# Optimization experiments

Hardware: AMD Instinct MI355X
Metric: run time of the kernel (lower is better)

Reference implementation:

```python
import jax, jax.numpy as jnp
import numpy as np

B, T, H = 4, 2048, 1024
NH = 16
HD = H // NH  # 64
NEG_INF = -1.0e9  # module uses -1e9, not -inf


def setup_inputs() -> dict:
    key = jax.random.key(0)
    k1, k2, k3 = jax.random.split(key, 3)
    x = jax.random.normal(k1, (B, T, H), dtype=jnp.float32)
    W_qkv = jax.random.normal(k2, (3 * H, H), dtype=jnp.float32) * (1.0 / np.sqrt(H))
    W_out = jax.random.normal(k3, (H, H), dtype=jnp.float32) * (1.0 / np.sqrt(H))
    return {"x": x, "W_qkv": W_qkv, "W_out": W_out}


def reference(x, W_qkv, W_out):
    Bx, Tx, C = x.shape
    qkv = x @ W_qkv.T                              # [B,T,3H]
    q, k, v = jnp.split(qkv, 3, axis=-1)
    # [B,T,H] -> [B,NH,T,HD]
    q = q.reshape(Bx, Tx, NH, HD).transpose(0, 2, 1, 3)
    k = k.reshape(Bx, Tx, NH, HD).transpose(0, 2, 1, 3)
    v = v.reshape(Bx, Tx, NH, HD).transpose(0, 2, 1, 3)
    scale = 1.0 / np.sqrt(HD)
    scores = jnp.einsum('bhqd,bhkd->bhqk', q, k) * scale  # [B,NH,T,T]
    causal = jnp.tril(jnp.ones((Tx, Tx), dtype=bool))[None, None]
    scores = jnp.where(causal, scores, jnp.asarray(NEG_INF, scores.dtype))
    attn = jax.nn.softmax(scores, axis=-1)
    out = jnp.einsum('bhqk,bhkd->bhqd', attn, v)   # [B,NH,T,HD]
    out = out.transpose(0, 2, 1, 3).reshape(Bx, Tx, C)
    return out @ W_out.T
```

## Files before the change

### kernel.cpp

```cpp
#include <hip/hip_runtime.h>
#include <hip/hip_bf16.h>


typedef unsigned short ushort_t;
typedef __attribute__((ext_vector_type(8))) short  s8v;
typedef __attribute__((ext_vector_type(4))) float  f4v;
typedef __attribute__((ext_vector_type(4))) unsigned int u4v;

__device__ inline ushort_t f2bf(float f) {
    unsigned u = __builtin_bit_cast(unsigned, f);
    u += 0x7fffu + ((u >> 16) & 1u);
    return (ushort_t)(u >> 16);
}

__device__ inline void gload16(const ushort_t* g, ushort_t* l) {
    __builtin_amdgcn_global_load_lds(
        (const __attribute__((address_space(1))) unsigned int*)g,
        (__attribute__((address_space(3))) unsigned int*)l, 16, 0, 0);
}

__global__ __launch_bounds__(256) void cast_f32_bf16(
    const float* __restrict__ in, ushort_t* __restrict__ out, int n8)
{
    int i = blockIdx.x * 256 + threadIdx.x;
    if (i >= n8) return;
    const float* p = in + (size_t)i * 8;
    f4v a = *(const f4v*)p;
    f4v b = *(const f4v*)(p + 4);
    union { u4v v; ushort_t u[8]; } o;
    #pragma unroll
    for (int j = 0; j < 4; j++) { o.u[j] = f2bf(a[j]); o.u[j + 4] = f2bf(b[j]); }
    *(u4v*)(out + (size_t)i * 8) = o.v;
}

__global__ __launch_bounds__(256) void transpose_v(
    const ushort_t* __restrict__ in, ushort_t* __restrict__ out)
{
    const int t0 = blockIdx.x * 64;
    const int bh = blockIdx.y;
    const ushort_t* src = in  + ((size_t)bh * 2048 + t0) * 64;
    ushort_t*       dst = out + (size_t)bh * 64 * 2048 + t0;
    __shared__ __align__(16) ushort_t L[64 * 72];
    const int tid = threadIdx.x;

    #pragma unroll
    for (int j = 0; j < 2; j++) {
        int c = tid + j * 256;
        int t = c >> 3, d0 = (c & 7) * 8;
        *(s8v*)&L[t * 72 + d0] = *(const s8v*)(src + (size_t)t * 64 + d0);
    }
    __syncthreads();
    #pragma unroll
    for (int j = 0; j < 2; j++) {
        int c = tid + j * 256;
        int d = c >> 3, sp0 = (c & 7) * 8;
        union { s8v v; ushort_t u[8]; } o;
        #pragma unroll
        for (int i = 0; i < 8; i++) {
            int sp = sp0 + i;
            int sl = sp & 31;
            int k  = (sp >> 5) * 32 + (sl & 1) * 16 + (sl >> 1);
            o.u[i] = L[k * 72 + d];
        }
        *(s8v*)(dst + (size_t)d * 2048 + sp0) = o.v;
    }
}

template<int MODE>
__global__ __launch_bounds__(256) void gemm_nt(
    const ushort_t* __restrict__ A, const ushort_t* __restrict__ Bm,
    ushort_t* __restrict__ o0, ushort_t* __restrict__ o1, ushort_t* __restrict__ o2,
    float* __restrict__ of)
{
    __shared__ __align__(16) ushort_t As[2][4096];
    __shared__ __align__(16) ushort_t Bs[2][4096];

    const int tid  = threadIdx.x;
    const int m0   = blockIdx.x * 128;
    const int n0   = blockIdx.y * 128;
    const int wave = tid >> 6, lane = tid & 63;
    const int wr = wave >> 1, wc = wave & 1;
    const int lhi = lane >> 4, llo = lane & 15;
    const int srow = lane >> 2;
    const int scol = (((lane & 3) ^ ((srow >> 1) & 3)) * 8);

    auto stage = [&](int k0, int buf) {
        #pragma unroll
        for (int p = 0; p < 2; p++) {
            int chunk = wave * 2 + p;
            int row = chunk * 16 + srow;
            gload16(A  + (size_t)(m0 + row) * 1024 + k0 + scol,
                    &As[buf][chunk * 512 + lane * 8]);
            gload16(Bm + (size_t)(n0 + row) * 1024 + k0 + scol,
                    &Bs[buf][chunk * 512 + lane * 8]);
        }
    };

    f4v acc[4][4] = {};
    int buf = 0;

    stage(0, 0);
    __syncthreads();

    for (int k0 = 0; k0 < 1024; k0 += 32) {
        if (k0 + 32 < 1024) stage(k0 + 32, buf ^ 1);

        const int rch = (lhi ^ ((llo >> 1) & 3)) * 8;
        s8v a[4], b[4];
        #pragma unroll
        for (int i = 0; i < 4; i++)
            a[i] = *(const s8v*)&As[buf][(wr * 64 + i * 16 + llo) * 32 + rch];
        #pragma unroll
        for (int i = 0; i < 4; i++)
            b[i] = *(const s8v*)&Bs[buf][(wc * 64 + i * 16 + llo) * 32 + rch];
        #pragma unroll
        for (int i = 0; i < 4; i++)
            #pragma unroll
            for (int j = 0; j < 4; j++)
                acc[i][j] = __builtin_amdgcn_mfma_f32_16x16x32_bf16(a[i], b[j], acc[i][j], 0, 0, 0);

        __syncthreads();
        buf ^= 1;
    }

    #pragma unroll
    for (int i = 0; i < 4; i++) {
        #pragma unroll
        for (int j = 0; j < 4; j++) {
            #pragma unroll
            for (int r = 0; r < 4; r++) {
                int m = m0 + wr * 64 + i * 16 + lhi * 4 + r;
                int n = n0 + wc * 64 + j * 16 + llo;
                if (MODE == 1) {
                    of[(size_t)m * 1024 + n] = acc[i][j][r];
                } else {
                    float val = acc[i][j][r];
                    int b  = m >> 11, t = m & 2047;
                    int which = n >> 10, hh = n & 1023;
                    int head = hh >> 6, d = hh & 63;
                    size_t bh = (size_t)(b * 16 + head);
                    if (which == 0)
                        o0[(size_t)m * 1024 + hh] = f2bf(val * 0.18033688011112042f);
                    else {
                        ushort_t* dst = (which == 1) ? o1 : o2;
                        dst[(bh * 2048 + t) * 64 + d] = f2bf(val);
                    }
                }
            }
        }
    }
}

__global__ __launch_bounds__(512, 4) void attn_kernel(
    const ushort_t* __restrict__ q_ws, const ushort_t* __restrict__ k_ws,
    const ushort_t* __restrict__ v_ws, ushort_t* __restrict__ ao_ws)
{
    const int p    = blockIdx.x;
    const int bh   = blockIdx.y;
    const int tid  = threadIdx.x;
    const int wave = tid >> 6, lane = tid & 63;
    const int lhi = lane >> 4, llo = lane & 15;
    const int b = bh >> 4, head = bh & 15;

    const ushort_t* Kb = k_ws + (size_t)bh * 2048 * 64;
    const ushort_t* Vb = v_ws + (size_t)bh * 64 * 2048;

    __shared__ __align__(16) ushort_t Ks [2][4096];
    __shared__ __align__(16) ushort_t Vts[2][4096];
    __shared__ __align__(16) ushort_t Ps [8][2][1280];

    const int srow = wave * 8 + (lane >> 3);
    const int gch  = ((lane & 7) ^ (srow & 7)) * 8;
    auto stage = [&](int t, int buf) {
        const int kk0 = t * 64;
        gload16(Kb + (size_t)(kk0 + srow) * 64 + gch,
                &Ks[buf][srow * 64 + (lane & 7) * 8]);
        gload16(Vb + (size_t)srow * 2048 + kk0 + gch,
                &Vts[buf][srow * 64 + (lane & 7) * 8]);
    };

    const int qt  = (wave >> 2) ? (15 - p) : p;
    const int wq0 = qt * 128 + (wave & 3) * 32;

    s8v qf[2][2];
    #pragma unroll
    for (int g = 0; g < 2; g++) {
        const ushort_t* Qp = q_ws + (size_t)(b * 2048 + wq0 + g * 16 + llo) * 1024 + head * 64;
        qf[g][0] = *(const s8v*)(Qp + lhi * 8);
        qf[g][1] = *(const s8v*)(Qp + 32 + lhi * 8);
    }

    f4v o[2][4] = {};
    float lsum[2][4] = {};

    const int ntb = 32 - 2 * p;
    const int xs  = llo & 7;
    int cur = 0;

    stage(0, 0);
    __syncthreads();

    #pragma unroll 1
    for (int t = 0; t < ntb; t++) {
        if (t + 1 < ntb) stage(t + 1, cur ^ 1);

        const int kk0 = t * 64;
        if (kk0 <= wq0 + 31) {
            f4v s0[4], s1[4];
            #pragma unroll
            for (int c = 0; c < 4; c++) {
                const int rb = (c * 16 + llo) * 64;
                s8v kb0 = *(const s8v*)&Ks[cur][rb + ((lhi    ) ^ xs) * 8];
                s8v kb1 = *(const s8v*)&Ks[cur][rb + ((4 + lhi) ^ xs) * 8];
                f4v z0 = {}, z1 = {};
                z0 = __builtin_amdgcn_mfma_f32_16x16x32_bf16(qf[0][0], kb0, z0, 0, 0, 0);
                z0 = __builtin_amdgcn_mfma_f32_16x16x32_bf16(qf[0][1], kb1, z0, 0, 0, 0);
                z1 = __builtin_amdgcn_mfma_f32_16x16x32_bf16(qf[1][0], kb0, z1, 0, 0, 0);
                z1 = __builtin_amdgcn_mfma_f32_16x16x32_bf16(qf[1][1], kb1, z1, 0, 0, 0);
                s0[c] = z0; s1[c] = z1;
            }

            #pragma unroll
            for (int g = 0; g < 2; g++) {
                const int qrb = wq0 + g * 16;
                f4v* s = g ? s1 : s0;
                if ((kk0 + 63) > qrb) {
                    #pragma unroll
                    for (int c = 0; c < 4; c++) {
                        int kkg = kk0 + c * 16 + llo;
                        #pragma unroll
                        for (int r = 0; r < 4; r++)
                            if (kkg > qrb + lhi * 4 + r) s[c][r] = -1e9f;
                    }
                }
                #pragma unroll
                for (int h = 0; h < 2; h++) {
                    #pragma unroll
                    for (int r = 0; r < 4; r++) {
                        float p0 = __builtin_amdgcn_exp2f(s[2 * h][r]);
                        float p1 = __builtin_amdgcn_exp2f(s[2 * h + 1][r]);
                        lsum[g][r] += p0 + p1;
                        unsigned pk;
                        asm("v_cvt_pk_bf16_f32 %0, %1, %2" : "=v"(pk) : "v"(p0), "v"(p1));
                        *(unsigned*)&Ps[wave][g][h * 640 + (lhi * 4 + r) * 40 + llo * 2] = pk;
                    }
                }
            }

            s8v pa[2][2];
            #pragma unroll
            for (int g = 0; g < 2; g++) {
                pa[g][0] = *(const s8v*)&Ps[wave][g][llo * 40 + lhi * 8];
                pa[g][1] = *(const s8v*)&Ps[wave][g][640 + llo * 40 + lhi * 8];
            }
            #pragma unroll
            for (int cd = 0; cd < 4; cd++) {
                const int rb = (cd * 16 + llo) * 64;
                s8v vb0 = *(const s8v*)&Vts[cur][rb + ((lhi    ) ^ xs) * 8];
                s8v vb1 = *(const s8v*)&Vts[cur][rb + ((4 + lhi) ^ xs) * 8];
                #pragma unroll
                for (int g = 0; g < 2; g++) {
                    o[g][cd] = __builtin_amdgcn_mfma_f32_16x16x32_bf16(pa[g][0], vb0, o[g][cd], 0, 0, 0);
                    o[g][cd] = __builtin_amdgcn_mfma_f32_16x16x32_bf16(pa[g][1], vb1, o[g][cd], 0, 0, 0);
                }
            }
        }

        __syncthreads();
        cur ^= 1;
    }

    #pragma unroll
    for (int off = 1; off < 16; off <<= 1)
        #pragma unroll
        for (int g = 0; g < 2; g++)
            #pragma unroll
            for (int r = 0; r < 4; r++)
                lsum[g][r] += __shfl_xor(lsum[g][r], off, 64);

    #pragma unroll
    for (int g = 0; g < 2; g++)
        #pragma unroll
        for (int cd = 0; cd < 4; cd++)
            #pragma unroll
            for (int r = 0; r < 4; r++) {
                int qq = wq0 + g * 16 + lhi * 4 + r;
                int d  = cd * 16 + llo;
                ao_ws[((size_t)(b * 2048 + qq)) * 1024 + head * 64 + d] =
                    f2bf(o[g][cd][r] / lsum[g][r]);
            }
}

extern "C" void kernel_launch(void* const* d_in, const int* in_sizes, int n_in,
                              void* d_out, int out_size, void* d_ws, size_t ws_size,
                              hipStream_t stream) {
    const float* x    = (const float*)d_in[0];
    const float* wqkv = (const float*)d_in[1];
    const float* wout = (const float*)d_in[2];

    ushort_t* wqkvb = (ushort_t*)d_ws;
    ushort_t* woutb = wqkvb + 3145728;
    ushort_t* xb    = woutb + 1048576;
    ushort_t* q_ws  = xb + 8388608;
    ushort_t* k_ws  = q_ws + 8388608;
    ushort_t* vt_ws = k_ws + 8388608;
    ushort_t* v_ws  = xb;
    ushort_t* ao_ws = vt_ws;
    float*    out   = (float*)d_out;

    cast_f32_bf16<<<4096, 256, 0, stream>>>(x,    xb,    1048576);
    cast_f32_bf16<<<1536, 256, 0, stream>>>(wqkv, wqkvb, 393216);
    cast_f32_bf16<<< 512, 256, 0, stream>>>(wout, woutb, 131072);
    gemm_nt<0><<<dim3(64, 24), 256, 0, stream>>>(xb, wqkvb, q_ws, k_ws, vt_ws, nullptr);
    transpose_v<<<dim3(32, 64), 256, 0, stream>>>(vt_ws, v_ws);
    attn_kernel<<<dim3(8, 64), 512, 0, stream>>>(q_ws, k_ws, v_ws, ao_ws);
    gemm_nt<1><<<dim3(64, 8), 256, 0, stream>>>(ao_ws, woutb, nullptr, nullptr, nullptr, out);
}
```

Before: 248.2 us.

## Replace QKV projection GEMM with 256x256-tile pipelined 8-wave kernel

Adds a dedicated QKV GEMM kernel that uses 256x256 output tiles, 512 threads and a double-buffered, XOR-swizzled LDS layout fed by direct global-to-LDS loads. The K loop is split into four quadrant phases, and each phase's loads are interleaved with MFMA work under raised wave priority. The larger tile is meant to raise arithmetic intensity and cut global and LDS traffic per FLOP relative to the 128x128 generic kernel. In exchange it uses 128KB of LDS per block and a 384-block grid, which can leave a partial wave of blocks on the CUs.

After: 256.7 us. +3.4%, slower.

```diff
diff --git a/kernel.cpp b/kernel.cpp
--- a/kernel.cpp
+++ b/kernel.cpp
@@ -64,6 +64,111 @@
         }
         *(s8v*)(dst + (size_t)d * 2048 + sp0) = o.v;
     }
+}
+
+__global__ __launch_bounds__(512, 2) void gemm256_qkv(
+    const ushort_t* __restrict__ A, const ushort_t* __restrict__ Bm,
+    ushort_t* __restrict__ o0, ushort_t* __restrict__ o1, ushort_t* __restrict__ o2)
+{
+    __shared__ __align__(16) ushort_t Ls[2][2][2][8192];
+
+    const int tid  = threadIdx.x;
+    const int m0   = blockIdx.x * 256;
+    const int n0   = blockIdx.y * 256;
+    const int wave = tid >> 6, lane = tid & 63;
+    const int wm = wave >> 2, wn = wave & 3;
+    const int lhi = lane >> 4, llo = lane & 15;
+    const int xs  = llo & 7;
+
+    auto stage = [&](int tile, int role) {
+        const int d    = tile & 1;
+        const int op   = (role == 1 || role == 2) ? 0 : 1;
+        const int half = (role >= 2) ? 1 : 0;
+        const ushort_t* base = op ? Bm : A;
+        const int r0 = op ? n0 : m0;
+        #pragma unroll
+        for (int rr = 0; rr < 2; rr++) {
+            int row = wave * 8 + (lane >> 3) + rr * 64;
+            int gch = ((lane & 7) ^ (row & 7)) * 8;
+            gload16(base + (size_t)(r0 + half * 128 + row) * 1024 + tile * 64 + gch,
+                    &Ls[d][op][half][row * 64 + (lane & 7) * 8]);
+        }
+    };
+
+    f4v acc[2][2][4][2] = {};
+
+    stage(0, 0); stage(0, 1); stage(0, 2); stage(0, 3);
+    stage(1, 0); stage(1, 1);
+    asm volatile("s_waitcnt vmcnt(4)" ::: "memory");
+    __builtin_amdgcn_s_barrier();
+
+#define GPHASE(D, QA, QB, ST, SR, VM) do {                                       \
+    s8v af[4][2], bf[2][2];                                                      \
+    _Pragma("unroll")                                                            \
+    for (int i = 0; i < 4; i++)                                                  \
+      _Pragma("unroll")                                                          \
+      for (int s = 0; s < 2; s++)                                                \
+        af[i][s] = *(const s8v*)&Ls[D][0][QA][(wm*64 + i*16 + llo)*64 + ((s*4 + lhi) ^ xs)*8]; \
+    _Pragma("unroll")                                                            \
+    for (int j = 0; j < 2; j++)                                                  \
+      _Pragma("unroll")                                                          \
+      for (int s = 0; s < 2; s++)                                                \
+        bf[j][s] = *(const s8v*)&Ls[D][1][QB][(wn*32 + j*16 + llo)*64 + ((s*4 + lhi) ^ xs)*8]; \
+    if ((ST) < 16) stage((ST), (SR));                                            \
+    __builtin_amdgcn_s_barrier();                                                \
+    __builtin_amdgcn_s_setprio(1);                                               \
+    _Pragma("unroll")                                                            \
+    for (int s = 0; s < 2; s++)                                                  \
+      _Pragma("unroll")                                                          \
+      for (int i = 0; i < 4; i++)                                                \
+        _Pragma("unroll")                                                        \
+        for (int j = 0; j < 2; j++)                                              \
+          acc[QA][QB][i][j] = __builtin_amdgcn_mfma_f32_16x16x32_bf16(af[i][s], bf[j][s], acc[QA][QB][i][j], 0, 0, 0); \
+    __builtin_amdgcn_s_setprio(0);                                               \
+    if ((VM) == 4)      asm volatile("s_waitcnt vmcnt(4)" ::: "memory");         \
+    else if ((VM) == 0) asm volatile("s_waitcnt vmcnt(0)" ::: "memory");         \
+    __builtin_amdgcn_s_barrier();                                                \
+  } while (0)
+
+    #pragma unroll 1
+    for (int it = 0; it < 8; ++it) {
+        const int s1 = it * 2 + 1, s2 = it * 2 + 2, s3 = it * 2 + 3;
+        const int vm = (it == 7) ? 0 : 4;
+        GPHASE(0, 0, 0, s1, 2, -1);
+        GPHASE(0, 1, 0, s1, 3, -1);
+        GPHASE(0, 0, 1, s2, 0, -1);
+        GPHASE(0, 1, 1, s2, 1, vm);
+        GPHASE(1, 0, 0, s2, 2, -1);
+        GPHASE(1, 1, 0, s2, 3, -1);
+        GPHASE(1, 0, 1, s3, 0, -1);
+        GPHASE(1, 1, 1, s3, 1, vm);
+    }
+#undef GPHASE
+
+    #pragma unroll
+    for (int qa = 0; qa < 2; qa++)
+    #pragma unroll
+    for (int qb = 0; qb < 2; qb++)
+    #pragma unroll
+    for (int i = 0; i < 4; i++)
+    #pragma unroll
+    for (int j = 0; j < 2; j++)
+        #pragma unroll
+        for (int r = 0; r < 4; r++) {
+            int m = m0 + qa * 128 + wm * 64 + i * 16 + lhi * 4 + r;
+            int n = n0 + qb * 128 + wn * 32 + j * 16 + llo;
+            float val = acc[qa][qb][i][j][r];
+            int b  = m >> 11, t = m & 2047;
+            int which = n >> 10, hh = n & 1023;
+            int head = hh >> 6, d = hh & 63;
+            size_t bh = (size_t)(b * 16 + head);
+            if (which == 0)
+                o0[(size_t)m * 1024 + hh] = f2bf(val * 0.18033688011112042f);
+            else {
+                ushort_t* dst = (which == 1) ? o1 : o2;
+                dst[(bh * 2048 + t) * 64 + d] = f2bf(val);
+            }
+        }
 }
 
 template<int MODE>
@@ -311,7 +416,7 @@
     cast_f32_bf16<<<4096, 256, 0, stream>>>(x,    xb,    1048576);
     cast_f32_bf16<<<1536, 256, 0, stream>>>(wqkv, wqkvb, 393216);
     cast_f32_bf16<<< 512, 256, 0, stream>>>(wout, woutb, 131072);
-    gemm_nt<0><<<dim3(64, 24), 256, 0, stream>>>(xb, wqkvb, q_ws, k_ws, vt_ws, nullptr);
+    gemm256_qkv<<<dim3(32, 12), 512, 0, stream>>>(xb, wqkvb, q_ws, k_ws, vt_ws);
     transpose_v<<<dim3(32, 64), 256, 0, stream>>>(vt_ws, v_ws);
     attn_kernel<<<dim3(8, 64), 512, 0, stream>>>(q_ws, k_ws, v_ws, ao_ws);
     gemm_nt<1><<<dim3(64, 8), 256, 0, stream>>>(ao_ws, woutb, nullptr, nullptr, nullptr, out);
```

## Fuse V transpose into QKV GEMM epilogue and merge cast kernels

Applied to the files above, without the earlier changes.

The three f32-to-bf16 cast launches become one kernel that picks its source by thread index. The separate V transpose kernel is removed, and the QKV GEMM blocks that produce V now stage their accumulators in shared memory and write the permuted transposed V layout directly. This drops one full round trip of V through global memory and several launches. In exchange, the V-producing blocks get extra shared-memory passes and barriers in their epilogue.

Result: faster. 228.7 us (-7.9%).

```diff
diff --git a/kernel.cpp b/kernel.cpp
--- a/kernel.cpp
+++ b/kernel.cpp
@@ -19,51 +19,23 @@
         (__attribute__((address_space(3))) unsigned int*)l, 16, 0, 0);
 }
 
-__global__ __launch_bounds__(256) void cast_f32_bf16(
-    const float* __restrict__ in, ushort_t* __restrict__ out, int n8)
+__global__ __launch_bounds__(256) void cast_all(
+    const float* __restrict__ x, const float* __restrict__ wqkv,
+    const float* __restrict__ wout, ushort_t* __restrict__ xb,
+    ushort_t* __restrict__ wqkvb, ushort_t* __restrict__ woutb)
 {
     int i = blockIdx.x * 256 + threadIdx.x;
-    if (i >= n8) return;
-    const float* p = in + (size_t)i * 8;
+    const float* src; ushort_t* dst; int off;
+    if (i < 1048576)      { src = x;    dst = xb;    off = i; }
+    else if (i < 1441792) { src = wqkv; dst = wqkvb; off = i - 1048576; }
+    else                  { src = wout; dst = woutb; off = i - 1441792; }
+    const float* p = src + (size_t)off * 8;
     f4v a = *(const f4v*)p;
     f4v b = *(const f4v*)(p + 4);
     union { u4v v; ushort_t u[8]; } o;
     #pragma unroll
     for (int j = 0; j < 4; j++) { o.u[j] = f2bf(a[j]); o.u[j + 4] = f2bf(b[j]); }
-    *(u4v*)(out + (size_t)i * 8) = o.v;
-}
-
-__global__ __launch_bounds__(256) void transpose_v(
-    const ushort_t* __restrict__ in, ushort_t* __restrict__ out)
-{
-    const int t0 = blockIdx.x * 64;
-    const int bh = blockIdx.y;
-    const ushort_t* src = in  + ((size_t)bh * 2048 + t0) * 64;
-    ushort_t*       dst = out + (size_t)bh * 64 * 2048 + t0;
-    __shared__ __align__(16) ushort_t L[64 * 72];
-    const int tid = threadIdx.x;
-
-    #pragma unroll
-    for (int j = 0; j < 2; j++) {
-        int c = tid + j * 256;
-        int t = c >> 3, d0 = (c & 7) * 8;
-        *(s8v*)&L[t * 72 + d0] = *(const s8v*)(src + (size_t)t * 64 + d0);
-    }
-    __syncthreads();
-    #pragma unroll
-    for (int j = 0; j < 2; j++) {
-        int c = tid + j * 256;
-        int d = c >> 3, sp0 = (c & 7) * 8;
-        union { s8v v; ushort_t u[8]; } o;
-        #pragma unroll
-        for (int i = 0; i < 8; i++) {
-            int sp = sp0 + i;
-            int sl = sp & 31;
-            int k  = (sp >> 5) * 32 + (sl & 1) * 16 + (sl >> 1);
-            o.u[i] = L[k * 72 + d];
-        }
-        *(s8v*)(dst + (size_t)d * 2048 + sp0) = o.v;
-    }
+    *(u4v*)(dst + (size_t)off * 8) = o.v;
 }
 
 template<int MODE>
@@ -72,8 +44,7 @@
     ushort_t* __restrict__ o0, ushort_t* __restrict__ o1, ushort_t* __restrict__ o2,
     float* __restrict__ of)
 {
-    __shared__ __align__(16) ushort_t As[2][4096];
-    __shared__ __align__(16) ushort_t Bs[2][4096];
+    __shared__ __align__(16) ushort_t SH[16384];
 
     const int tid  = threadIdx.x;
     const int m0   = blockIdx.x * 128;
@@ -90,9 +61,9 @@
             int chunk = wave * 2 + p;
             int row = chunk * 16 + srow;
             gload16(A  + (size_t)(m0 + row) * 1024 + k0 + scol,
-                    &As[buf][chunk * 512 + lane * 8]);
+                    &SH[buf * 4096 + chunk * 512 + lane * 8]);
             gload16(Bm + (size_t)(n0 + row) * 1024 + k0 + scol,
-                    &Bs[buf][chunk * 512 + lane * 8]);
+                    &SH[8192 + buf * 4096 + chunk * 512 + lane * 8]);
         }
     };
 
@@ -109,10 +80,10 @@
         s8v a[4], b[4];
         #pragma unroll
         for (int i = 0; i < 4; i++)
-            a[i] = *(const s8v*)&As[buf][(wr * 64 + i * 16 + llo) * 32 + rch];
+            a[i] = *(const s8v*)&SH[buf * 4096 + (wr * 64 + i * 16 + llo) * 32 + rch];
         #pragma unroll
         for (int i = 0; i < 4; i++)
-            b[i] = *(const s8v*)&Bs[buf][(wc * 64 + i * 16 + llo) * 32 + rch];
+            b[i] = *(const s8v*)&SH[8192 + buf * 4096 + (wc * 64 + i * 16 + llo) * 32 + rch];
         #pragma unroll
         for (int i = 0; i < 4; i++)
             #pragma unroll
@@ -121,6 +92,45 @@
 
         __syncthreads();
         buf ^= 1;
+    }
+
+    if (MODE == 0 && n0 >= 2048) {
+        const int hbase = (n0 - 2048) >> 6;
+        const int t0b   = m0 & 2047;
+        const int bb    = m0 >> 11;
+        #pragma unroll 1
+        for (int p = 0; p < 2; p++) {
+            __syncthreads();
+            if (wr == p) {
+                #pragma unroll
+                for (int i = 0; i < 4; i++)
+                    #pragma unroll
+                    for (int j = 0; j < 4; j++) {
+                        union { unsigned long long q; ushort_t u[4]; } w;
+                        #pragma unroll
+                        for (int r = 0; r < 4; r++) w.u[r] = f2bf(acc[i][j][r]);
+                        int nrel = wc * 64 + j * 16 + llo;
+                        *(unsigned long long*)&SH[nrel * 68 + i * 16 + lhi * 4] = w.q;
+                    }
+            }
+            __syncthreads();
+            #pragma unroll
+            for (int cc = 0; cc < 4; cc++) {
+                int c  = cc * 256 + tid;
+                int nn = c >> 3, sp0 = (c & 7) * 8;
+                union { s8v v; ushort_t u[8]; } o;
+                #pragma unroll
+                for (int i2 = 0; i2 < 8; i2++) {
+                    int sp = sp0 + i2;
+                    int k  = ((sp >> 5) << 5) | ((sp & 1) << 4) | ((sp & 31) >> 1);
+                    o.u[i2] = SH[nn * 68 + k];
+                }
+                int head = hbase + (nn >> 6), d = nn & 63;
+                size_t bh = (size_t)(bb * 16 + head);
+                *(s8v*)(o2 + ((bh * 64 + d) * 2048 + t0b + p * 64 + sp0)) = o.v;
+            }
+        }
+        return;
     }
 
     #pragma unroll
@@ -141,10 +151,8 @@
                     size_t bh = (size_t)(b * 16 + head);
                     if (which == 0)
                         o0[(size_t)m * 1024 + hh] = f2bf(val * 0.18033688011112042f);
-                    else {
-                        ushort_t* dst = (which == 1) ? o1 : o2;
-                        dst[(bh * 2048 + t) * 64 + d] = f2bf(val);
-                    }
+                    else
+                        o1[(bh * 2048 + t) * 64 + d] = f2bf(val);
                 }
             }
         }
@@ -303,16 +311,12 @@
     ushort_t* xb    = woutb + 1048576;
     ushort_t* q_ws  = xb + 8388608;
     ushort_t* k_ws  = q_ws + 8388608;
-    ushort_t* vt_ws = k_ws + 8388608;
-    ushort_t* v_ws  = xb;
-    ushort_t* ao_ws = vt_ws;
+    ushort_t* v_ws  = k_ws + 8388608;
+    ushort_t* ao_ws = xb;
     float*    out   = (float*)d_out;
 
-    cast_f32_bf16<<<4096, 256, 0, stream>>>(x,    xb,    1048576);
-    cast_f32_bf16<<<1536, 256, 0, stream>>>(wqkv, wqkvb, 393216);
-    cast_f32_bf16<<< 512, 256, 0, stream>>>(wout, woutb, 131072);
-    gemm_nt<0><<<dim3(64, 24), 256, 0, stream>>>(xb, wqkvb, q_ws, k_ws, vt_ws, nullptr);
-    transpose_v<<<dim3(32, 64), 256, 0, stream>>>(vt_ws, v_ws);
+    cast_all<<<6144, 256, 0, stream>>>(x, wqkv, wout, xb, wqkvb, woutb);
+    gemm_nt<0><<<dim3(64, 24), 256, 0, stream>>>(xb, wqkvb, q_ws, k_ws, v_ws, nullptr);
     attn_kernel<<<dim3(8, 64), 512, 0, stream>>>(q_ws, k_ws, v_ws, ao_ws);
     gemm_nt<1><<<dim3(64, 8), 256, 0, stream>>>(ao_ws, woutb, nullptr, nullptr, nullptr, out);
 }
```
